# Kernel tuning notes

Measured on AMD Instinct MI355X. Metric: run time of the kernel, lower is better.

## Reference

```python
import jax, jax.numpy as jnp
import numpy as np

KS = 5  # kernel_size


def _conv(x, w, b):
    # valid cross-correlation, same math as unfold + w.view matmul + fold
    y = jax.lax.conv_general_dilated(
        x, w, window_strides=(1, 1), padding='VALID',
        dimension_numbers=('NCHW', 'OIHW', 'NCHW'))
    return y + b


def _avgpool2(x):
    # non-overlapping 2x2 average pool (unfold(2,2,stride=2) + mean over patch)
    B, C, H, W = x.shape
    return x.reshape(B, C, H // 2, 2, W // 2, 2).mean(axis=(3, 5))


def setup_inputs() -> dict:
    key = jax.random.key(0)
    ks = jax.random.split(key, 8)
    h1, h2 = 10, 20
    L1n, L2n, L3n, out_n = 4 * 4 * h2, 120, 84, 10

    def xavier(k, shape, fan_in, fan_out):
        std = np.sqrt(2.0 / (fan_in + fan_out))
        return jax.random.normal(k, shape, dtype=jnp.float32) * std

    x = jax.random.normal(ks[0], (8192, 1, 28, 28), dtype=jnp.float32)
    W1 = xavier(ks[1], (h1, 1, KS, KS), 1 * KS * KS, h1 * KS * KS)
    b1 = jnp.zeros((1, h1, 1, 1), jnp.float32)
    W2 = xavier(ks[2], (h2, h1, KS, KS), h1 * KS * KS, h2 * KS * KS)
    b2 = jnp.zeros((1, h2, 1, 1), jnp.float32)
    L1 = jax.random.normal(ks[3], (L1n, L2n), dtype=jnp.float32)
    Lb1 = jnp.zeros((1, L2n), jnp.float32)
    L2 = jax.random.normal(ks[4], (L2n, L3n), dtype=jnp.float32)
    Lb2 = jnp.zeros((1, L3n), jnp.float32)
    L3 = jax.random.normal(ks[5], (L3n, out_n), dtype=jnp.float32)
    Lb3 = jnp.zeros((1, out_n), jnp.float32)
    return {'x': x, 'W1': W1, 'b1': b1, 'W2': W2, 'b2': b2,
            'L1': L1, 'Lb1': Lb1, 'L2': L2, 'Lb2': Lb2, 'L3': L3, 'Lb3': Lb3}


def reference(x, W1, b1, W2, b2, L1, Lb1, L2, Lb2, L3, Lb3):
    h = jax.nn.sigmoid(_avgpool2(_conv(x, W1, b1)))      # [B,10,12,12]
    h = jax.nn.sigmoid(_avgpool2(_conv(h, W2, b2)))      # [B,20,4,4]
    h = h.reshape(h.shape[0], -1)                        # [B,320]
    h = jax.nn.sigmoid(h @ L1 + Lb1)                     # [B,120]
    h = jax.nn.sigmoid(h @ L2 + Lb2)                     # [B,84]
    return h @ L3 + Lb3                                  # [B,10]
```

## Files before the change

kernel.cpp:

```cpp
#include <hip/hip_runtime.h>
#include <math.h>


__device__ __forceinline__ float sigf(float v) {
    return 1.0f / (1.0f + __expf(-v));
}

__global__ void k_prep(const float* __restrict__ W1, const float* __restrict__ W2,
                       float* __restrict__ w6, float* __restrict__ w2q) {
    int i = blockIdx.x * 256 + threadIdx.x;
    if (i < 5000) {
        int kx = i % 5, t = i / 5;
        int ky = t % 5, t2 = t / 5;
        int ic = t2 % 10, c = t2 / 10;
        w2q[((ic * 5 + ky) * 20 + c) * 5 + kx] = W2[i];
    }
    int k = i - 5000;
    if (k >= 0 && k < 480) {
        int kx = k % 8, t = k / 8;
        int c = t % 10, ky = t / 10;
        float v = 0.f;
        if (kx < 6) {
            for (int dy = 0; dy < 2; ++dy)
                for (int dx = 0; dx < 2; ++dx) {
                    int sy = ky - dy, sx = kx - dx;
                    if (sy >= 0 && sy < 5 && sx >= 0 && sx < 5)
                        v += W1[c * 25 + sy * 5 + sx];
                }
        }
        w6[k] = v;
    }
}

__global__ __launch_bounds__(512) void k_conv1(
    const float* __restrict__ x, const float* __restrict__ w6g,
    const float* __restrict__ b1, float* __restrict__ S1g) {
    __shared__ float4 XR[8 * 224];
    __shared__ float wq1[480];
    __shared__ float bs1[10];

    const int tid = threadIdx.x;
    const long img0 = (long)blockIdx.x * 8;

    {
        const float4* xg = (const float4*)(x + img0 * 784);
        for (int i = tid; i < 1568; i += 512) {
            int im = i / 196, j = i % 196, r = j / 7, kk = j % 7;
            XR[im * 224 + r * 8 + (kk ^ ((r >> 1) & 7))] = xg[i];
        }
    }
    if (tid < 480) wq1[tid] = w6g[tid];
    else if (tid < 490) bs1[tid - 480] = b1[tid - 480];
    __syncthreads();

    const int im = tid >> 6, l = tid & 63;
    const long img = img0 + im;
    if (l < 60) {
        const int cc = l / 12, py = l % 12, ch0 = cc * 2;
        float acc0[12], acc1[12];
#pragma unroll
        for (int p = 0; p < 12; ++p) { acc0[p] = 0.f; acc1[p] = 0.f; }

        const float4* xr = &XR[im * 224];
#pragma unroll
        for (int ky = 0; ky < 6; ++ky) {
            const int r = 2 * py + ky;
            const int hsh = (r >> 1) & 7;
            const int base = r * 8;
            union { float4 v[7]; float f[28]; } R;
#pragma unroll
            for (int q = 0; q < 7; ++q) R.v[q] = xr[base + (q ^ hsh)];
            union { float4 v[2]; float f[8]; } W0, W1;
            const float* wb = &wq1[(ky * 10 + ch0) * 8];
            W0.v[0] = *(const float4*)(wb);
            W0.v[1] = *(const float4*)(wb + 4);
            W1.v[0] = *(const float4*)(wb + 8);
            W1.v[1] = *(const float4*)(wb + 12);
#pragma unroll
            for (int kx = 0; kx < 6; ++kx) {
                const float w0 = W0.f[kx], w1 = W1.f[kx];
#pragma unroll
                for (int px = 0; px < 12; ++px) {
                    const float xv = R.f[2 * px + kx];
                    acc0[px] += xv * w0;
                    acc1[px] += xv * w1;
                }
            }
        }

#define FINISH_CH(ACC, CH)                                                   \
        {                                                                    \
            float h[12];                                                     \
            _Pragma("unroll")                                                \
            for (int px = 0; px < 12; ++px)                                  \
                h[px] = sigf(ACC[px] * 0.25f + bs1[CH]);                     \
            float hh[11];                                                    \
            _Pragma("unroll")                                                \
            for (int t = 0; t < 11; ++t) hh[t] = h[t] + h[t + 1];            \
            float o[12];                                                     \
            _Pragma("unroll")                                                \
            for (int t = 0; t < 11; ++t)                                     \
                o[t] = hh[t] + __shfl_down(hh[t], 1, 64);                    \
            o[11] = 0.f;                                                     \
            if (py < 11) {                                                   \
                float* sp = S1g + img * 1320 + (CH) * 132 + py * 12;         \
                ((float4*)sp)[0] = make_float4(o[0], o[1], o[2], o[3]);      \
                ((float4*)sp)[1] = make_float4(o[4], o[5], o[6], o[7]);      \
                ((float4*)sp)[2] = make_float4(o[8], o[9], o[10], o[11]);    \
            }                                                                \
        }
        FINISH_CH(acc0, ch0)
        FINISH_CH(acc1, ch0 + 1)
#undef FINISH_CH
    }
}

__global__ __launch_bounds__(320) void k_conv2(
    const float* __restrict__ S1g, const float* __restrict__ w2qg,
    const float* __restrict__ b2, float* __restrict__ h2) {
    const int w = threadIdx.x >> 6, l = threadIdx.x & 63;
    const int cg = __builtin_amdgcn_readfirstlane(w);
    const int im = l >> 3, py = (l >> 1) & 3, xh = l & 1;
    const long img0 = (long)blockIdx.x * 8;

    float acc[4][2];
#pragma unroll
    for (int a = 0; a < 4; ++a) { acc[a][0] = 0.f; acc[a][1] = 0.f; }

    const float* s1 = S1g + (img0 + im) * 1320;
    const float* wg = w2qg + cg * 20;
    for (int ic = 0; ic < 10; ++ic) {
#pragma unroll
        for (int ky = 0; ky < 5; ++ky) {
            const int ro = ic * 132 + (2 * py + ky) * 12 + xh * 4;
            union { float4 v[2]; float f[8]; } R;
            R.v[0] = *(const float4*)(s1 + ro);
            R.v[1] = *(const float4*)(s1 + ro + 4);
            const float* wrow = wg + (ic * 5 + ky) * 100;
#pragma unroll
            for (int cc = 0; cc < 4; ++cc)
#pragma unroll
                for (int kx = 0; kx < 5; ++kx) {
                    const float wv = wrow[cc * 5 + kx];
                    acc[cc][0] += R.f[kx] * wv;
                    acc[cc][1] += R.f[2 + kx] * wv;
                }
        }
    }

    float* outp = h2 + (img0 + im) * 320 + (cg * 4) * 16 + py * 4 + xh * 2;
#pragma unroll
    for (int cc = 0; cc < 4; ++cc) {
        const float bv = b2[cg * 4 + cc];
        float2 o;
        o.x = sigf(acc[cc][0] * 0.25f + bv);
        o.y = sigf(acc[cc][1] * 0.25f + bv);
        *(float2*)(outp + cc * 16) = o;
    }
}

#define TSTR 18
__global__ __launch_bounds__(256) void k_fc(
    const float* __restrict__ h2, const float* __restrict__ L1,
    const float* __restrict__ Lb1, const float* __restrict__ L2,
    const float* __restrict__ Lb2, const float* __restrict__ L3,
    const float* __restrict__ Lb3, float* __restrict__ out) {
    __shared__ float arena[18480];
    float* h2t = arena;
    float* wt  = arena + 5760;
    float* g1t = arena + 13952;
    float* g2t = arena + 16112;
    float* L3s = arena + 17624;

    const int tid = threadIdx.x;
    const long img0 = (long)blockIdx.x * 16;

    for (int i = tid; i < 1280; i += 256) {
        const int im = i / 80, fq = i % 80;
        float4 v = *(const float4*)(h2 + (img0 + im) * 320 + fq * 4);
        h2t[(fq * 4 + 0) * TSTR + im] = v.x;
        h2t[(fq * 4 + 1) * TSTR + im] = v.y;
        h2t[(fq * 4 + 2) * TSTR + im] = v.z;
        h2t[(fq * 4 + 3) * TSTR + im] = v.w;
    }
#pragma unroll
    for (int r = 0; r < 4; ++r) {
        const int idx = tid + 256 * r, row = idx >> 5, c4 = idx & 31;
        if (c4 < 30)
            *(float4*)(wt + row * 128 + c4 * 4) =
                *(const float4*)(L1 + row * 120 + c4 * 4);
    }
    __syncthreads();

    const int p = tid >> 5, jg = tid & 31;
    const int jc = jg < 30 ? jg : 29;

    float acc[4][2];
    {
        union { float4 v; float f[4]; } bv;
        bv.v = *(const float4*)(Lb1 + jc * 4);
#pragma unroll
        for (int q = 0; q < 4; ++q) { acc[q][0] = bv.f[q]; acc[q][1] = bv.f[q]; }
    }
    int cur = 0;
    for (int t = 0; t < 10; ++t) {
        float4 wr0, wr1, wr2, wr3;
        if (t < 9) {
            const int k0n = (t + 1) * 32;
            const int c0 = tid & 31;
            wr0 = (c0 < 30) ? *(const float4*)(L1 + (k0n + (tid >> 5)) * 120 + c0 * 4) : make_float4(0, 0, 0, 0);
            wr1 = (c0 < 30) ? *(const float4*)(L1 + (k0n + ((tid + 256) >> 5)) * 120 + c0 * 4) : make_float4(0, 0, 0, 0);
            wr2 = (c0 < 30) ? *(const float4*)(L1 + (k0n + ((tid + 512) >> 5)) * 120 + c0 * 4) : make_float4(0, 0, 0, 0);
            wr3 = (c0 < 30) ? *(const float4*)(L1 + (k0n + ((tid + 768) >> 5)) * 120 + c0 * 4) : make_float4(0, 0, 0, 0);
        }
        const float* wb = wt + cur * 4096;
        const int kb = t * 32;
#pragma unroll
        for (int k = 0; k < 32; ++k) {
            union { float4 v; float f[4]; } w;
            w.v = *(const float4*)(wb + k * 128 + jc * 4);
            const float2 h = *(const float2*)&h2t[(kb + k) * TSTR + p * 2];
#pragma unroll
            for (int q = 0; q < 4; ++q) {
                acc[q][0] += w.f[q] * h.x;
                acc[q][1] += w.f[q] * h.y;
            }
        }
        if (t < 9) {
            float* wd = wt + (cur ^ 1) * 4096;
            const int c0 = tid & 31;
            if (c0 < 30) {
                *(float4*)(wd + (tid >> 5) * 128 + c0 * 4) = wr0;
                *(float4*)(wd + ((tid + 256) >> 5) * 128 + c0 * 4) = wr1;
                *(float4*)(wd + ((tid + 512) >> 5) * 128 + c0 * 4) = wr2;
                *(float4*)(wd + ((tid + 768) >> 5) * 128 + c0 * 4) = wr3;
            }
            cur ^= 1;
        }
        __syncthreads();
    }
    if (jg < 30) {
#pragma unroll
        for (int q = 0; q < 4; ++q) {
            g1t[(jg * 4 + q) * TSTR + p * 2 + 0] = sigf(acc[q][0]);
            g1t[(jg * 4 + q) * TSTR + p * 2 + 1] = sigf(acc[q][1]);
        }
    }
    __syncthreads();

    for (int i = tid; i < 2520; i += 256) {
        const int row = i / 21, c4 = i % 21;
        *(float4*)(arena + row * 88 + c4 * 4) =
            *(const float4*)(L2 + row * 84 + c4 * 4);
    }
    for (int i = tid; i < 840; i += 256) L3s[i] = L3[i];
    if (tid < 10) L3s[840 + tid] = Lb3[tid];
    __syncthreads();

    if (jg < 21) {
        union { float4 v; float f[4]; } bv;
        bv.v = *(const float4*)(Lb2 + jg * 4);
        float a2[4][2];
#pragma unroll
        for (int q = 0; q < 4; ++q) { a2[q][0] = bv.f[q]; a2[q][1] = bv.f[q]; }
#pragma unroll 4
        for (int k = 0; k < 120; ++k) {
            union { float4 v; float f[4]; } w;
            w.v = *(const float4*)(arena + k * 88 + jg * 4);
            const float2 h = *(const float2*)&g1t[k * TSTR + p * 2];
#pragma unroll
            for (int q = 0; q < 4; ++q) {
                a2[q][0] += w.f[q] * h.x;
                a2[q][1] += w.f[q] * h.y;
            }
        }
#pragma unroll
        for (int q = 0; q < 4; ++q) {
            g2t[(jg * 4 + q) * TSTR + p * 2 + 0] = sigf(a2[q][0]);
            g2t[(jg * 4 + q) * TSTR + p * 2 + 1] = sigf(a2[q][1]);
        }
    }
    __syncthreads();

    if (tid < 160) {
        const int im = tid / 10, j = tid % 10;
        float a = L3s[840 + j];
#pragma unroll 4
        for (int i = 0; i < 84; ++i)
            a += g2t[i * TSTR + im] * L3s[i * 10 + j];
        out[(img0 + im) * 10 + j] = a;
    }
}

extern "C" void kernel_launch(void* const* d_in, const int* in_sizes, int n_in,
                              void* d_out, int out_size, void* d_ws, size_t ws_size,
                              hipStream_t stream) {
    const float* x   = (const float*)d_in[0];
    const float* W1  = (const float*)d_in[1];
    const float* b1  = (const float*)d_in[2];
    const float* W2  = (const float*)d_in[3];
    const float* b2  = (const float*)d_in[4];
    const float* L1  = (const float*)d_in[5];
    const float* Lb1 = (const float*)d_in[6];
    const float* L2  = (const float*)d_in[7];
    const float* Lb2 = (const float*)d_in[8];
    const float* L3  = (const float*)d_in[9];
    const float* Lb3 = (const float*)d_in[10];
    float* out = (float*)d_out;

    const int B = in_sizes[0] / 784;

    char* ws = (char*)d_ws;
    float* w6  = (float*)ws;
    float* w2q = (float*)(ws + 4096);
    float* S1g = (float*)(ws + 4096 + 32768);
    float* h2  = (float*)(ws + 4096 + 32768 + (size_t)B * 1320 * 4);

    hipLaunchKernelGGL(k_prep, dim3(22), dim3(256), 0, stream, W1, W2, w6, w2q);
    hipLaunchKernelGGL(k_conv1, dim3(B / 8), dim3(512), 0, stream, x, w6, b1, S1g);
    hipLaunchKernelGGL(k_conv2, dim3(B / 8), dim3(320), 0, stream, S1g, w2q, b2, h2);
    hipLaunchKernelGGL(k_fc, dim3(B / 16), dim3(256), 0, stream,
                       h2, L1, Lb1, L2, Lb2, L3, Lb3, out);
}
```

Baseline: 92.78 us.

## Store conv1 intermediate as fp16 and reverse conv2 block order

The conv1 output buffer S1 is now stored as half precision with a per-image stride padded to 1328 elements. conv2 loads it as packed halves and converts to float, which halves the memory traffic for the intermediate. conv2 also visits image blocks in reverse group order, so it starts on data conv1 wrote most recently and may still find it in cache. Storing in fp16 loses precision in the intermediate activations.

```diff
diff --git a/kernel.cpp b/kernel.cpp
--- a/kernel.cpp
+++ b/kernel.cpp
@@ -1,4 +1,5 @@
 #include <hip/hip_runtime.h>
+#include <hip/hip_fp16.h>
 #include <math.h>
 
 
@@ -32,9 +33,11 @@
     }
 }
 
+#define S1IM 1328
+
 __global__ __launch_bounds__(512) void k_conv1(
     const float* __restrict__ x, const float* __restrict__ w6g,
-    const float* __restrict__ b1, float* __restrict__ S1g) {
+    const float* __restrict__ b1, __half* __restrict__ S1h) {
     __shared__ float4 XR[8 * 224];
     __shared__ float wq1[480];
     __shared__ float bs1[10];
@@ -103,10 +106,13 @@
                 o[t] = hh[t] + __shfl_down(hh[t], 1, 64);                    \
             o[11] = 0.f;                                                     \
             if (py < 11) {                                                   \
-                float* sp = S1g + img * 1320 + (CH) * 132 + py * 12;         \
-                ((float4*)sp)[0] = make_float4(o[0], o[1], o[2], o[3]);      \
-                ((float4*)sp)[1] = make_float4(o[4], o[5], o[6], o[7]);      \
-                ((float4*)sp)[2] = make_float4(o[8], o[9], o[10], o[11]);    \
+                union { __half hs[12]; uint2 u2[3]; } P;                     \
+                _Pragma("unroll")                                            \
+                for (int t = 0; t < 12; ++t) P.hs[t] = __float2half(o[t]);   \
+                __half* sp = S1h + img * S1IM + (CH) * 132 + py * 12;        \
+                ((uint2*)sp)[0] = P.u2[0];                                   \
+                ((uint2*)sp)[1] = P.u2[1];                                   \
+                ((uint2*)sp)[2] = P.u2[2];                                   \
             }                                                                \
         }
         FINISH_CH(acc0, ch0)
@@ -116,26 +122,35 @@
 }
 
 __global__ __launch_bounds__(320) void k_conv2(
-    const float* __restrict__ S1g, const float* __restrict__ w2qg,
+    const __half* __restrict__ S1h, const float* __restrict__ w2qg,
     const float* __restrict__ b2, float* __restrict__ h2) {
     const int w = threadIdx.x >> 6, l = threadIdx.x & 63;
     const int cg = __builtin_amdgcn_readfirstlane(w);
     const int im = l >> 3, py = (l >> 1) & 3, xh = l & 1;
-    const long img0 = (long)blockIdx.x * 8;
+    const int grp = gridDim.x / 8;
+    const int bidr = ((grp - 1 - ((int)blockIdx.x >> 3)) << 3) | ((int)blockIdx.x & 7);
+    const long img0 = (long)bidr * 8;
 
     float acc[4][2];
 #pragma unroll
     for (int a = 0; a < 4; ++a) { acc[a][0] = 0.f; acc[a][1] = 0.f; }
 
-    const float* s1 = S1g + (img0 + im) * 1320;
+    const __half* s1 = S1h + (img0 + im) * S1IM;
     const float* wg = w2qg + cg * 20;
     for (int ic = 0; ic < 10; ++ic) {
 #pragma unroll
         for (int ky = 0; ky < 5; ++ky) {
-            const int ro = ic * 132 + (2 * py + ky) * 12 + xh * 4;
+            const __half* rp = s1 + ic * 132 + (2 * py + ky) * 12 + xh * 4;
+            union { uint2 u; __half2 h2v[2]; } A, B;
+            A.u = *(const uint2*)(rp);
+            B.u = *(const uint2*)(rp + 4);
             union { float4 v[2]; float f[8]; } R;
-            R.v[0] = *(const float4*)(s1 + ro);
-            R.v[1] = *(const float4*)(s1 + ro + 4);
+            float2 f0 = __half22float2(A.h2v[0]);
+            float2 f1 = __half22float2(A.h2v[1]);
+            float2 f2 = __half22float2(B.h2v[0]);
+            float2 f3 = __half22float2(B.h2v[1]);
+            R.f[0] = f0.x; R.f[1] = f0.y; R.f[2] = f1.x; R.f[3] = f1.y;
+            R.f[4] = f2.x; R.f[5] = f2.y; R.f[6] = f3.x; R.f[7] = f3.y;
             const float* wrow = wg + (ic * 5 + ky) * 100;
 #pragma unroll
             for (int cc = 0; cc < 4; ++cc)
@@ -311,14 +326,14 @@
     const int B = in_sizes[0] / 784;
 
     char* ws = (char*)d_ws;
-    float* w6  = (float*)ws;
-    float* w2q = (float*)(ws + 4096);
-    float* S1g = (float*)(ws + 4096 + 32768);
-    float* h2  = (float*)(ws + 4096 + 32768 + (size_t)B * 1320 * 4);
+    float* w6   = (float*)ws;
+    float* w2q  = (float*)(ws + 4096);
+    __half* S1h = (__half*)(ws + 4096 + 32768);
+    float* h2   = (float*)(ws + 4096 + 32768 + (size_t)B * S1IM * 2);
 
     hipLaunchKernelGGL(k_prep, dim3(22), dim3(256), 0, stream, W1, W2, w6, w2q);
-    hipLaunchKernelGGL(k_conv1, dim3(B / 8), dim3(512), 0, stream, x, w6, b1, S1g);
-    hipLaunchKernelGGL(k_conv2, dim3(B / 8), dim3(320), 0, stream, S1g, w2q, b2, h2);
+    hipLaunchKernelGGL(k_conv1, dim3(B / 8), dim3(512), 0, stream, x, w6, b1, S1h);
+    hipLaunchKernelGGL(k_conv2, dim3(B / 8), dim3(320), 0, stream, S1h, w2q, b2, h2);
     hipLaunchKernelGGL(k_fc, dim3(B / 16), dim3(256), 0, stream,
                        h2, L1, Lb1, L2, Lb2, L3, Lb3, out);
 }
```

Result: faster. 90.43 us (-2.5%).
